# Kernel optimization log

Measured on AMD Instinct MI355X. Metric: run time of the kernel, lower is better.

Reference implementation:

```python
import jax, jax.numpy as jnp
import numpy as np

B, S, H, NH = 2, 2048, 1024, 16
D = H // NH  # per-head dim = 64
NEG = -1000000000.0
EPS = 1e-6


def setup_inputs() -> dict:
    key = jax.random.key(0)
    ks = jax.random.split(key, 8)
    q = jax.random.normal(ks[0], (B, S, H), dtype=jnp.float32)
    k = jax.random.normal(ks[1], (B, S, H), dtype=jnp.float32)
    v = jax.random.normal(ks[2], (B, S, H), dtype=jnp.float32)
    mask = jax.random.randint(ks[3], (B, S, S), 0, 2, dtype=jnp.int32)
    # learned params (torch Linear stores W as [out,in]; y = x @ W.T)
    sc = 1.0 / np.sqrt(H)
    Wq = jax.random.normal(ks[4], (H, H), dtype=jnp.float32) * sc
    Wk = jax.random.normal(ks[5], (H, H), dtype=jnp.float32) * sc
    Wv = jax.random.normal(ks[6], (H, H), dtype=jnp.float32) * sc
    ln_gamma = jnp.ones((H,), dtype=jnp.float32)
    ln_beta = jnp.zeros((H,), dtype=jnp.float32)
    return {"q": q, "k": k, "v": v, "mask": mask,
            "Wq": Wq, "Wk": Wk, "Wv": Wv,
            "ln_gamma": ln_gamma, "ln_beta": ln_beta}


def _mha(q, k, v, mask, Wq, Wk, Wv, ln_gamma, ln_beta):
    residual = q
    # projections: note original never applies self.scale, and self.fc is unused
    qh = (q @ Wq.T).reshape(B, S, NH, D).transpose(0, 2, 1, 3)  # [B,NH,S,D]
    kh = (k @ Wk.T).reshape(B, S, NH, D).transpose(0, 2, 1, 3)
    vh = (v @ Wv.T).reshape(B, S, NH, D).transpose(0, 2, 1, 3)
    scores = jnp.einsum('bhqd,bhkd->bhqk', qh, kh)  # NO 1/sqrt(d) scaling (faithful)
    scores = jnp.where(mask[:, None, :, :] == 0, NEG, scores)
    attn = jax.nn.softmax(scores, axis=-1)
    ctx = jnp.einsum('bhqk,bhkd->bhqd', attn, vh)
    ctx = ctx.transpose(0, 2, 1, 3).reshape(B, S, H)
    ctx = ctx + residual  # dropout = identity in eval
    mu = jnp.mean(ctx, axis=-1, keepdims=True)
    var = jnp.var(ctx, axis=-1, keepdims=True)
    out = (ctx - mu) / jnp.sqrt(var + EPS) * ln_gamma + ln_beta
    return out, attn


def reference(q, k, v, mask, Wq, Wk, Wv, ln_gamma, ln_beta):
    return _mha(q, k, v, mask, Wq, Wk, Wv, ln_gamma, ln_beta)
```

## Files before the change

kernel.cpp:

```cpp
#include <hip/hip_runtime.h>
#include <hip/hip_fp16.h>

typedef _Float16 f16;
typedef _Float16 f16x8 __attribute__((ext_vector_type(8)));
typedef _Float16 f16x4 __attribute__((ext_vector_type(4)));
typedef float    f32x4 __attribute__((ext_vector_type(4)));
typedef float    f32x2 __attribute__((ext_vector_type(2)));

#define NEGV -1000000000.0f

__global__ __launch_bounds__(256) void cvt3(const float* __restrict__ a,
                                            const float* __restrict__ b,
                                            const float* __restrict__ c,
                                            f16* __restrict__ out, int per) {
  const float* src = blockIdx.y == 0 ? a : (blockIdx.y == 1 ? b : c);
  int i = (blockIdx.x * 256 + threadIdx.x) * 4;
  if (i >= per) return;
  f32x4 v = *(const f32x4*)(src + i);
  f16x4 h; h[0]=(f16)v[0]; h[1]=(f16)v[1]; h[2]=(f16)v[2]; h[3]=(f16)v[3];
  *(f16x4*)(out + (size_t)blockIdx.y * per + i) = h;
}

__global__ __launch_bounds__(256) void pack_mask(const int* __restrict__ m,
                                                 unsigned* __restrict__ bits) {
  size_t i = (size_t)blockIdx.x * 256 + threadIdx.x;
  unsigned long long b = __ballot(m[i] != 0);
  int lane = threadIdx.x & 63;
  if (lane == 0)       bits[i >> 5] = (unsigned)b;
  else if (lane == 32) bits[i >> 5] = (unsigned)(b >> 32);
}

__device__ inline void gld16(const void* g, void* l) {
  __builtin_amdgcn_global_load_lds((const __attribute__((address_space(1))) void*)g,
                                   (__attribute__((address_space(3))) void*)l, 16, 0, 0);
}

__global__ __launch_bounds__(256) void gemm_proj(const f16* __restrict__ Xall,
                                                 const f16* __restrict__ Wall,
                                                 f16* __restrict__ Qh,
                                                 f16* __restrict__ Kh,
                                                 f16* __restrict__ Vn) {
  __shared__ f16 lA[4][128][8];
  __shared__ f16 lB[4][128][8];
  const int z = blockIdx.z;
  const f16* A  = Xall + (size_t)z * (4096u * 1024u);
  const f16* Wt = Wall + (size_t)z * (1024u * 1024u);
  f16* Y = (z == 0) ? Qh : (z == 1 ? Kh : Vn);
  const int t = threadIdx.x;
  const int brow = blockIdx.y * 128, bcol = blockIdx.x * 128;
  const int w = t >> 6, l = t & 63;
  const int wr = w >> 1, wc = w & 1;
  const int lr = l & 15, lg = l >> 4;
  f32x4 acc[4][4] = {};

  for (int k0 = 0; k0 < 1024; k0 += 32) {
#pragma unroll
    for (int j = 0; j < 2; j++) {
      const int p = j * 4096 + t * 16;
      const int ks = p >> 11, row = (p >> 4) & 127;
      gld16(A  + (size_t)(brow + row) * 1024 + k0 + ks * 8, (char*)lA + p);
      gld16(Wt + (size_t)(bcol + row) * 1024 + k0 + ks * 8, (char*)lB + p);
    }
    __syncthreads();
    f16x8 af[4], bf[4];
#pragma unroll
    for (int mi = 0; mi < 4; mi++) af[mi] = *(const f16x8*)&lA[lg][wr * 64 + mi * 16 + lr][0];
#pragma unroll
    for (int ni = 0; ni < 4; ni++) bf[ni] = *(const f16x8*)&lB[lg][wc * 64 + ni * 16 + lr][0];
#pragma unroll
    for (int mi = 0; mi < 4; mi++)
#pragma unroll
      for (int ni = 0; ni < 4; ni++)
        acc[mi][ni] = __builtin_amdgcn_mfma_f32_16x16x32_f16(af[mi], bf[ni], acc[mi][ni], 0, 0, 0);
    __syncthreads();
  }

  const int mb0 = brow + wr * 64, nb0 = bcol + wc * 64;
#pragma unroll
  for (int mi = 0; mi < 4; mi++)
#pragma unroll
    for (int ni = 0; ni < 4; ni++)
#pragma unroll
      for (int j = 0; j < 4; j++) {
        const int m = mb0 + mi * 16 + lg * 4 + j;
        const int n = nb0 + ni * 16 + lr;
        const int bb = m >> 11, s = m & 2047;
        const int h = n >> 6, d = n & 63;
        Y[((((size_t)bb * 16 + h) * 2048 + s) << 6) + d] = (f16)acc[mi][ni][j];
      }
}

__global__ __launch_bounds__(512) void transposeV(const f16* __restrict__ Vn,
                                                  f16* __restrict__ VhT) {
  const int bh = blockIdx.y, s0 = blockIdx.x * 64;
  const int t = threadIdx.x, l = t & 63, w = t >> 6;
  const f16x8 v = *(const f16x8*)(Vn + (((size_t)bh * 2048 + s0 + l) << 6) + w * 8);
#pragma unroll
  for (int e = 0; e < 8; e++)
    VhT[(((size_t)bh * 64 + w * 8 + e) << 11) + s0 + l] = v[e];
}

__device__ inline char* swzW(char* wb, int row, int col) {
  return wb + row * 256 + ((col * 2) ^ ((row & 7) << 4));
}

__global__ __launch_bounds__(512, 4) void attn_fused(const f16* __restrict__ Qh,
                                                     const f16* __restrict__ Kh,
                                                     const f16* __restrict__ VhT,
                                                     const unsigned* __restrict__ mbits,
                                                     float* __restrict__ attn,
                                                     float* __restrict__ ctx) {
  __shared__ f16 lK[8][128][8];
  __shared__ f16 lVT[16][64][8];
  __shared__ char Pw[8 * 4096];
  const int wg = blockIdx.x;
  const int bh = (wg >> 1) & 31;
  const int qg = ((wg >> 6) << 1) | (wg & 1);
  const int b = bh >> 4, h = bh & 15;
  const int t = threadIdx.x, w = t >> 6, l = t & 63;
  const int lr = l & 15, lg = l >> 4;
  const int qr = qg * 128 + w * 16;
  char* wb = Pw + w * 4096;

  const int pA = t * 16, pB = 8192 + t * 16;
  const int ksA = pA >> 11, rwA = (pA >> 4) & 127;
  const int ksB = pB >> 11, rwB = (pB >> 4) & 127;
  const int vsA = pA >> 10, vdA = (pA >> 4) & 63;
  const int vsB = pB >> 10, vdB = (pB >> 4) & 63;
  const f16* Kbase = Kh + ((size_t)bh << 17);
  const f16* Vbase = VhT + ((size_t)bh << 17);

  const f16* qp = Qh + (((size_t)bh * 2048 + qr + lr) << 6) + lg * 8;
  const f16x8 aq0 = *(const f16x8*)qp;
  const f16x8 aq1 = *(const f16x8*)(qp + 32);

  const unsigned* mrow0 = mbits + ((size_t)b * 2048 + qr + lg * 4) * 64;

  float sj[4] = {0.f, 0.f, 0.f, 0.f};
  f16x8 kra = *(const f16x8*)(Kbase + ((size_t)rwA << 6) + ksA * 8);
  f16x8 krb = *(const f16x8*)(Kbase + ((size_t)rwB << 6) + ksB * 8);
  for (int t16 = 0; t16 < 16; t16++) {
    const int kb = t16 * 128;
    __syncthreads();
    *(f16x8*)((char*)lK + pA) = kra;
    *(f16x8*)((char*)lK + pB) = krb;
    __syncthreads();
    uint4 mrow[4];
#pragma unroll
    for (int j = 0; j < 4; j++) mrow[j] = *(const uint4*)(mrow0 + j * 64 + (kb >> 5));
    if (t16 < 15) {
      const f16* nb = Kbase + ((size_t)(kb + 128) << 6);
      kra = *(const f16x8*)(nb + ((size_t)rwA << 6) + ksA * 8);
      krb = *(const f16x8*)(nb + ((size_t)rwB << 6) + ksB * 8);
    }
#pragma unroll
    for (int nf = 0; nf < 8; nf++) {
      f32x4 s4 = {};
      s4 = __builtin_amdgcn_mfma_f32_16x16x32_f16(aq0, *(const f16x8*)&lK[lg][nf * 16 + lr][0], s4, 0, 0, 0);
      s4 = __builtin_amdgcn_mfma_f32_16x16x32_f16(aq1, *(const f16x8*)&lK[4 + lg][nf * 16 + lr][0], s4, 0, 0, 0);
      const unsigned bp = ((nf & 1) << 4) + lr;
#pragma unroll
      for (int j = 0; j < 4; j++) {
        const unsigned bit = (((const unsigned*)&mrow[j])[nf >> 1] >> bp) & 1u;
        sj[j] += bit ? __expf(s4[j]) : 0.f;
      }
    }
  }
  float SI[4];
#pragma unroll
  for (int j = 0; j < 4; j++) {
    float s = sj[j];
#pragma unroll
    for (int o = 1; o < 16; o <<= 1) s += __shfl_xor(s, o, 64);
    SI[j] = 1.0f / s;
  }

  f32x4 acc[4] = {};
  kra = *(const f16x8*)(Kbase + ((size_t)rwA << 6) + ksA * 8);
  krb = *(const f16x8*)(Kbase + ((size_t)rwB << 6) + ksB * 8);
  f16x8 vra = *(const f16x8*)(Vbase + ((size_t)vdA << 11) + vsA * 8);
  f16x8 vrb = *(const f16x8*)(Vbase + ((size_t)vdB << 11) + vsB * 8);
  float* abase = attn + (((size_t)bh * 2048 + qr) << 11);
  const int srow = l >> 3, scol = (l & 7) * 4;
  for (int t16 = 0; t16 < 16; t16++) {
    const int kb = t16 * 128;
    __syncthreads();
    *(f16x8*)((char*)lK + pA) = kra;
    *(f16x8*)((char*)lK + pB) = krb;
    *(f16x8*)((char*)lVT + pA) = vra;
    *(f16x8*)((char*)lVT + pB) = vrb;
    __syncthreads();
    uint4 mrow[4];
#pragma unroll
    for (int j = 0; j < 4; j++) mrow[j] = *(const uint4*)(mrow0 + j * 64 + (kb >> 5));
    if (t16 < 15) {
      const f16* nk = Kbase + ((size_t)(kb + 128) << 6);
      kra = *(const f16x8*)(nk + ((size_t)rwA << 6) + ksA * 8);
      krb = *(const f16x8*)(nk + ((size_t)rwB << 6) + ksB * 8);
      const f16* nv = Vbase + kb + 128;
      vra = *(const f16x8*)(nv + ((size_t)vdA << 11) + vsA * 8);
      vrb = *(const f16x8*)(nv + ((size_t)vdB << 11) + vsB * 8);
    }
#pragma unroll
    for (int nf = 0; nf < 8; nf++) {
      f32x4 s4 = {};
      s4 = __builtin_amdgcn_mfma_f32_16x16x32_f16(aq0, *(const f16x8*)&lK[lg][nf * 16 + lr][0], s4, 0, 0, 0);
      s4 = __builtin_amdgcn_mfma_f32_16x16x32_f16(aq1, *(const f16x8*)&lK[4 + lg][nf * 16 + lr][0], s4, 0, 0, 0);
      const unsigned bp = ((nf & 1) << 4) + lr;
#pragma unroll
      for (int j = 0; j < 4; j++) {
        const unsigned bit = (((const unsigned*)&mrow[j])[nf >> 1] >> bp) & 1u;
        const float pj = bit ? __expf(s4[j]) * SI[j] : 0.f;
        *(f16*)swzW(wb, lg * 4 + j, nf * 16 + lr) = (f16)pj;
      }
    }
#pragma unroll
    for (int kk = 0; kk < 4; kk++) {
      const f16x8 pa = *(const f16x8*)swzW(wb, lr, kk * 32 + lg * 8);
#pragma unroll
      for (int nf = 0; nf < 4; nf++)
        acc[nf] = __builtin_amdgcn_mfma_f32_16x16x32_f16(pa, *(const f16x8*)&lVT[kk * 4 + lg][nf * 16 + lr][0], acc[nf], 0, 0, 0);
    }
#pragma unroll
    for (int h2 = 0; h2 < 2; h2++) {
      const int row = srow + h2 * 8;
      float* arow = abase + ((size_t)row << 11) + kb + scol;
#pragma unroll
      for (int u = 0; u < 4; u++) {
        const f16x4 p4 = *(const f16x4*)swzW(wb, row, scol + u * 32);
        f32x4 o;
#pragma unroll
        for (int e = 0; e < 4; e++) o[e] = (float)p4[e];
        *(f32x4*)(arow + u * 32) = o;
      }
    }
  }

#pragma unroll
  for (int nf = 0; nf < 4; nf++)
#pragma unroll
    for (int j = 0; j < 4; j++)
      ctx[((size_t)b * 2048 + qr + lg * 4 + j) * 1024 + h * 64 + nf * 16 + lr] = acc[nf][j];
}

__global__ __launch_bounds__(256) void ln_res(const float* __restrict__ qres,
                                              const float* __restrict__ gamma,
                                              const float* __restrict__ beta,
                                              float* __restrict__ io) {
  const int tok = blockIdx.x;
  const int t = threadIdx.x;
  float* rowp = io + (size_t)tok * 1024;
  const float* qp = qres + (size_t)tok * 1024;
  const f32x4 c = *(const f32x4*)(rowp + t * 4);
  const f32x4 r = *(const f32x4*)(qp + t * 4);
  f32x4 vals;
  float s = 0.f, s2 = 0.f;
#pragma unroll
  for (int e = 0; e < 4; e++) { float x = c[e] + r[e]; vals[e] = x; s += x; s2 += x * x; }
#pragma unroll
  for (int o = 1; o < 64; o <<= 1) { s += __shfl_xor(s, o, 64); s2 += __shfl_xor(s2, o, 64); }
  __shared__ float rs[4][2];
  const int w = t >> 6;
  if ((t & 63) == 0) { rs[w][0] = s; rs[w][1] = s2; }
  __syncthreads();
  s  = rs[0][0] + rs[1][0] + rs[2][0] + rs[3][0];
  s2 = rs[0][1] + rs[1][1] + rs[2][1] + rs[3][1];
  const float mu = s * (1.f / 1024.f);
  const float var = s2 * (1.f / 1024.f) - mu * mu;
  const float rstd = rsqrtf(var + 1e-6f);
  const f32x4 g  = *(const f32x4*)(gamma + t * 4);
  const f32x4 be = *(const f32x4*)(beta + t * 4);
  f32x4 o;
#pragma unroll
  for (int e = 0; e < 4; e++) o[e] = (vals[e] - mu) * rstd * g[e] + be[e];
  *(f32x4*)(rowp + t * 4) = o;
}

extern "C" void kernel_launch(void* const* d_in, const int* in_sizes, int n_in,
                              void* d_out, int out_size, void* d_ws, size_t ws_size,
                              hipStream_t stream) {
  const float* q     = (const float*)d_in[0];
  const float* k     = (const float*)d_in[1];
  const float* v     = (const float*)d_in[2];
  const int*   mask  = (const int*)d_in[3];
  const float* Wq    = (const float*)d_in[4];
  const float* Wk    = (const float*)d_in[5];
  const float* Wv    = (const float*)d_in[6];
  const float* gamma = (const float*)d_in[7];
  const float* beta  = (const float*)d_in[8];
  float* out  = (float*)d_out;
  float* attn = out + (size_t)4194304;
  const size_t MB = 1u << 20;
  char* ws = (char*)d_ws;

  f16 *x16, *W16, *Qh, *Kh, *Vn, *VhT; unsigned* mb;
  if (ws_size >= 63 * MB) {
    x16 = (f16*)ws;              W16 = (f16*)(ws + 24 * MB);
    Qh  = (f16*)(ws + 30 * MB);  Kh  = (f16*)(ws + 38 * MB);
    Vn  = (f16*)(ws + 46 * MB);  VhT = (f16*)(ws + 54 * MB);
    mb  = (unsigned*)(ws + 62 * MB);
  } else {
    x16 = (f16*)attn;            W16 = (f16*)((char*)attn + 24 * MB);
    Vn  = (f16*)((char*)attn + 30 * MB);
    Qh  = (f16*)ws;              Kh  = (f16*)(ws + 8 * MB);
    VhT = (f16*)(ws + 16 * MB);  mb  = (unsigned*)(ws + 24 * MB);
  }

  cvt3<<<dim3(4096, 3), 256, 0, stream>>>(q, k, v, x16, 4194304);
  cvt3<<<dim3(1024, 3), 256, 0, stream>>>(Wq, Wk, Wv, W16, 1048576);
  pack_mask<<<dim3(32768), 256, 0, stream>>>(mask, mb);
  gemm_proj<<<dim3(8, 32, 3), 256, 0, stream>>>(x16, W16, Qh, Kh, Vn);
  transposeV<<<dim3(32, 32), 512, 0, stream>>>(Vn, VhT);
  attn_fused<<<dim3(512), 512, 0, stream>>>(Qh, Kh, VhT, mb, attn, out);
  ln_res<<<dim3(4096), 256, 0, stream>>>(q, gamma, beta, out);
}
```

Baseline: 332.2 us.

## Load K/V MFMA operands directly from global memory, drop LDS staging and barriers

Removes the shared-memory staging of K and V tiles and the two block-wide barriers per iteration. Each wave now reads its MFMA B operands straight from global memory and relies on L2/cache reuse across the eight waves. It also remaps workgroup-to-(batch,head,query-group) indexing so that blocks sharing the same head run close together. This trades LDS traffic and synchronisation for more global/L2 load traffic and exposed load latency with no explicit prefetch.

New measurement: 537.7 us. 61.9% more time.

```diff
diff --git a/kernel.cpp b/kernel.cpp
--- a/kernel.cpp
+++ b/kernel.cpp
@@ -110,23 +110,16 @@
                                                      const unsigned* __restrict__ mbits,
                                                      float* __restrict__ attn,
                                                      float* __restrict__ ctx) {
-  __shared__ f16 lK[8][128][8];
-  __shared__ f16 lVT[16][64][8];
   __shared__ char Pw[8 * 4096];
   const int wg = blockIdx.x;
-  const int bh = (wg >> 1) & 31;
-  const int qg = ((wg >> 6) << 1) | (wg & 1);
+  const int bh = ((wg & 7) << 2) | (wg >> 7);
+  const int qg = (wg >> 3) & 15;
   const int b = bh >> 4, h = bh & 15;
   const int t = threadIdx.x, w = t >> 6, l = t & 63;
   const int lr = l & 15, lg = l >> 4;
   const int qr = qg * 128 + w * 16;
   char* wb = Pw + w * 4096;
 
-  const int pA = t * 16, pB = 8192 + t * 16;
-  const int ksA = pA >> 11, rwA = (pA >> 4) & 127;
-  const int ksB = pB >> 11, rwB = (pB >> 4) & 127;
-  const int vsA = pA >> 10, vdA = (pA >> 4) & 63;
-  const int vsB = pB >> 10, vdB = (pB >> 4) & 63;
   const f16* Kbase = Kh + ((size_t)bh << 17);
   const f16* Vbase = VhT + ((size_t)bh << 17);
 
@@ -137,27 +130,20 @@
   const unsigned* mrow0 = mbits + ((size_t)b * 2048 + qr + lg * 4) * 64;
 
   float sj[4] = {0.f, 0.f, 0.f, 0.f};
-  f16x8 kra = *(const f16x8*)(Kbase + ((size_t)rwA << 6) + ksA * 8);
-  f16x8 krb = *(const f16x8*)(Kbase + ((size_t)rwB << 6) + ksB * 8);
   for (int t16 = 0; t16 < 16; t16++) {
     const int kb = t16 * 128;
-    __syncthreads();
-    *(f16x8*)((char*)lK + pA) = kra;
-    *(f16x8*)((char*)lK + pB) = krb;
-    __syncthreads();
     uint4 mrow[4];
 #pragma unroll
     for (int j = 0; j < 4; j++) mrow[j] = *(const uint4*)(mrow0 + j * 64 + (kb >> 5));
-    if (t16 < 15) {
-      const f16* nb = Kbase + ((size_t)(kb + 128) << 6);
-      kra = *(const f16x8*)(nb + ((size_t)rwA << 6) + ksA * 8);
-      krb = *(const f16x8*)(nb + ((size_t)rwB << 6) + ksB * 8);
-    }
+    const f16* kt = Kbase + ((size_t)(kb + lr) << 6) + lg * 8;
 #pragma unroll
     for (int nf = 0; nf < 8; nf++) {
+      const f16* kp = kt + (nf << 10);
+      const f16x8 bk0 = *(const f16x8*)kp;
+      const f16x8 bk1 = *(const f16x8*)(kp + 32);
       f32x4 s4 = {};
-      s4 = __builtin_amdgcn_mfma_f32_16x16x32_f16(aq0, *(const f16x8*)&lK[lg][nf * 16 + lr][0], s4, 0, 0, 0);
-      s4 = __builtin_amdgcn_mfma_f32_16x16x32_f16(aq1, *(const f16x8*)&lK[4 + lg][nf * 16 + lr][0], s4, 0, 0, 0);
+      s4 = __builtin_amdgcn_mfma_f32_16x16x32_f16(aq0, bk0, s4, 0, 0, 0);
+      s4 = __builtin_amdgcn_mfma_f32_16x16x32_f16(aq1, bk1, s4, 0, 0, 0);
       const unsigned bp = ((nf & 1) << 4) + lr;
 #pragma unroll
       for (int j = 0; j < 4; j++) {
@@ -176,36 +162,22 @@
   }
 
   f32x4 acc[4] = {};
-  kra = *(const f16x8*)(Kbase + ((size_t)rwA << 6) + ksA * 8);
-  krb = *(const f16x8*)(Kbase + ((size_t)rwB << 6) + ksB * 8);
-  f16x8 vra = *(const f16x8*)(Vbase + ((size_t)vdA << 11) + vsA * 8);
-  f16x8 vrb = *(const f16x8*)(Vbase + ((size_t)vdB << 11) + vsB * 8);
   float* abase = attn + (((size_t)bh * 2048 + qr) << 11);
   const int srow = l >> 3, scol = (l & 7) * 4;
   for (int t16 = 0; t16 < 16; t16++) {
     const int kb = t16 * 128;
-    __syncthreads();
-    *(f16x8*)((char*)lK + pA) = kra;
-    *(f16x8*)((char*)lK + pB) = krb;
-    *(f16x8*)((char*)lVT + pA) = vra;
-    *(f16x8*)((char*)lVT + pB) = vrb;
-    __syncthreads();
     uint4 mrow[4];
 #pragma unroll
     for (int j = 0; j < 4; j++) mrow[j] = *(const uint4*)(mrow0 + j * 64 + (kb >> 5));
-    if (t16 < 15) {
-      const f16* nk = Kbase + ((size_t)(kb + 128) << 6);
-      kra = *(const f16x8*)(nk + ((size_t)rwA << 6) + ksA * 8);
-      krb = *(const f16x8*)(nk + ((size_t)rwB << 6) + ksB * 8);
-      const f16* nv = Vbase + kb + 128;
-      vra = *(const f16x8*)(nv + ((size_t)vdA << 11) + vsA * 8);
-      vrb = *(const f16x8*)(nv + ((size_t)vdB << 11) + vsB * 8);
-    }
+    const f16* kt = Kbase + ((size_t)(kb + lr) << 6) + lg * 8;
 #pragma unroll
     for (int nf = 0; nf < 8; nf++) {
+      const f16* kp = kt + (nf << 10);
+      const f16x8 bk0 = *(const f16x8*)kp;
+      const f16x8 bk1 = *(const f16x8*)(kp + 32);
       f32x4 s4 = {};
-      s4 = __builtin_amdgcn_mfma_f32_16x16x32_f16(aq0, *(const f16x8*)&lK[lg][nf * 16 + lr][0], s4, 0, 0, 0);
-      s4 = __builtin_amdgcn_mfma_f32_16x16x32_f16(aq1, *(const f16x8*)&lK[4 + lg][nf * 16 + lr][0], s4, 0, 0, 0);
+      s4 = __builtin_amdgcn_mfma_f32_16x16x32_f16(aq0, bk0, s4, 0, 0, 0);
+      s4 = __builtin_amdgcn_mfma_f32_16x16x32_f16(aq1, bk1, s4, 0, 0, 0);
       const unsigned bp = ((nf & 1) << 4) + lr;
 #pragma unroll
       for (int j = 0; j < 4; j++) {
@@ -218,8 +190,10 @@
     for (int kk = 0; kk < 4; kk++) {
       const f16x8 pa = *(const f16x8*)swzW(wb, lr, kk * 32 + lg * 8);
 #pragma unroll
-      for (int nf = 0; nf < 4; nf++)
-        acc[nf] = __builtin_amdgcn_mfma_f32_16x16x32_f16(pa, *(const f16x8*)&lVT[kk * 4 + lg][nf * 16 + lr][0], acc[nf], 0, 0, 0);
+      for (int nf = 0; nf < 4; nf++) {
+        const f16x8 bv = *(const f16x8*)(Vbase + (((size_t)(nf * 16 + lr)) << 11) + kb + kk * 32 + lg * 8);
+        acc[nf] = __builtin_amdgcn_mfma_f32_16x16x32_f16(pa, bv, acc[nf], 0, 0, 0);
+      }
     }
 #pragma unroll
     for (int h2 = 0; h2 < 2; h2++) {
```

## Split attention into separate sum-exp kernel and PV/attn-write kernel

Applied to the files above, without the earlier changes.

The fused attention kernel ran two passes: first accumulating masked exp sums per row, then computing normalized probabilities, writing attn and doing the PV product. This splits the first pass into its own kernel that stores reciprocal row sums to workspace, and the second kernel reads them. It also changes the block-to-(bh,qg) mapping so consecutive blocks spread across heads. The intent is probably to reduce per-kernel register/LDS pressure or improve scheduling, at the cost of an extra launch and a small workspace round-trip.

Result: faster. 307.3 us (-7.5%).

```diff
diff --git a/kernel.cpp b/kernel.cpp
--- a/kernel.cpp
+++ b/kernel.cpp
@@ -100,22 +100,88 @@
     VhT[(((size_t)bh * 64 + w * 8 + e) << 11) + s0 + l] = v[e];
 }
 
+__global__ __launch_bounds__(512, 4) void sumexp_k(const f16* __restrict__ Qh,
+                                                   const f16* __restrict__ Kh,
+                                                   const unsigned* __restrict__ mbits,
+                                                   float* __restrict__ SIo) {
+  __shared__ f16 lK[8][128][8];
+  const int wg = blockIdx.x;
+  const int bh = ((wg & 7) << 2) | (wg >> 7);
+  const int qg = (wg >> 3) & 15;
+  const int b = bh >> 4;
+  const int t = threadIdx.x, w = t >> 6, l = t & 63;
+  const int lr = l & 15, lg = l >> 4;
+  const int qr = qg * 128 + w * 16;
+
+  const int pA = t * 16, pB = 8192 + t * 16;
+  const int ksA = pA >> 11, rwA = (pA >> 4) & 127;
+  const int ksB = pB >> 11, rwB = (pB >> 4) & 127;
+  const f16* Kbase = Kh + ((size_t)bh << 17);
+
+  const f16* qp = Qh + (((size_t)bh * 2048 + qr + lr) << 6) + lg * 8;
+  const f16x8 aq0 = *(const f16x8*)qp;
+  const f16x8 aq1 = *(const f16x8*)(qp + 32);
+  const unsigned* mrow0 = mbits + ((size_t)b * 2048 + qr + lg * 4) * 64;
+
+  float sj[4] = {0.f, 0.f, 0.f, 0.f};
+  f16x8 kra = *(const f16x8*)(Kbase + ((size_t)rwA << 6) + ksA * 8);
+  f16x8 krb = *(const f16x8*)(Kbase + ((size_t)rwB << 6) + ksB * 8);
+  for (int t16 = 0; t16 < 16; t16++) {
+    const int kb = t16 * 128;
+    __syncthreads();
+    *(f16x8*)((char*)lK + pA) = kra;
+    *(f16x8*)((char*)lK + pB) = krb;
+    __syncthreads();
+    uint4 mrow[4];
+#pragma unroll
+    for (int j = 0; j < 4; j++) mrow[j] = *(const uint4*)(mrow0 + j * 64 + (kb >> 5));
+    if (t16 < 15) {
+      const f16* nb = Kbase + ((size_t)(kb + 128) << 6);
+      kra = *(const f16x8*)(nb + ((size_t)rwA << 6) + ksA * 8);
+      krb = *(const f16x8*)(nb + ((size_t)rwB << 6) + ksB * 8);
+    }
+#pragma unroll
+    for (int nf = 0; nf < 8; nf++) {
+      f32x4 s4 = {};
+      s4 = __builtin_amdgcn_mfma_f32_16x16x32_f16(aq0, *(const f16x8*)&lK[lg][nf * 16 + lr][0], s4, 0, 0, 0);
+      s4 = __builtin_amdgcn_mfma_f32_16x16x32_f16(aq1, *(const f16x8*)&lK[4 + lg][nf * 16 + lr][0], s4, 0, 0, 0);
+      const unsigned bp = ((nf & 1) << 4) + lr;
+#pragma unroll
+      for (int j = 0; j < 4; j++) {
+        const unsigned bit = (((const unsigned*)&mrow[j])[nf >> 1] >> bp) & 1u;
+        sj[j] += bit ? __expf(s4[j]) : 0.f;
+      }
+    }
+  }
+#pragma unroll
+  for (int j = 0; j < 4; j++) {
+#pragma unroll
+    for (int o = 1; o < 16; o <<= 1) sj[j] += __shfl_xor(sj[j], o, 64);
+  }
+  if (lr == 0) {
+    float* o = SIo + ((size_t)bh << 11) + qr + lg * 4;
+    o[0] = 1.0f / sj[0]; o[1] = 1.0f / sj[1];
+    o[2] = 1.0f / sj[2]; o[3] = 1.0f / sj[3];
+  }
+}
+
 __device__ inline char* swzW(char* wb, int row, int col) {
   return wb + row * 256 + ((col * 2) ^ ((row & 7) << 4));
 }
 
-__global__ __launch_bounds__(512, 4) void attn_fused(const f16* __restrict__ Qh,
-                                                     const f16* __restrict__ Kh,
-                                                     const f16* __restrict__ VhT,
-                                                     const unsigned* __restrict__ mbits,
-                                                     float* __restrict__ attn,
-                                                     float* __restrict__ ctx) {
+__global__ __launch_bounds__(512, 4) void attn_pv(const f16* __restrict__ Qh,
+                                                  const f16* __restrict__ Kh,
+                                                  const f16* __restrict__ VhT,
+                                                  const unsigned* __restrict__ mbits,
+                                                  const float* __restrict__ SIo,
+                                                  float* __restrict__ attn,
+                                                  float* __restrict__ ctx) {
   __shared__ f16 lK[8][128][8];
   __shared__ f16 lVT[16][64][8];
   __shared__ char Pw[8 * 4096];
   const int wg = blockIdx.x;
-  const int bh = (wg >> 1) & 31;
-  const int qg = ((wg >> 6) << 1) | (wg & 1);
+  const int bh = ((wg & 7) << 2) | (wg >> 7);
+  const int qg = (wg >> 3) & 15;
   const int b = bh >> 4, h = bh & 15;
   const int t = threadIdx.x, w = t >> 6, l = t & 63;
   const int lr = l & 15, lg = l >> 4;
@@ -133,51 +199,15 @@
   const f16* qp = Qh + (((size_t)bh * 2048 + qr + lr) << 6) + lg * 8;
   const f16x8 aq0 = *(const f16x8*)qp;
   const f16x8 aq1 = *(const f16x8*)(qp + 32);
-
   const unsigned* mrow0 = mbits + ((size_t)b * 2048 + qr + lg * 4) * 64;
 
-  float sj[4] = {0.f, 0.f, 0.f, 0.f};
+  float SI[4];
+#pragma unroll
+  for (int j = 0; j < 4; j++) SI[j] = SIo[((size_t)bh << 11) + qr + lg * 4 + j];
+
+  f32x4 acc[4] = {};
   f16x8 kra = *(const f16x8*)(Kbase + ((size_t)rwA << 6) + ksA * 8);
   f16x8 krb = *(const f16x8*)(Kbase + ((size_t)rwB << 6) + ksB * 8);
-  for (int t16 = 0; t16 < 16; t16++) {
-    const int kb = t16 * 128;
-    __syncthreads();
-    *(f16x8*)((char*)lK + pA) = kra;
-    *(f16x8*)((char*)lK + pB) = krb;
-    __syncthreads();
-    uint4 mrow[4];
-#pragma unroll
-    for (int j = 0; j < 4; j++) mrow[j] = *(const uint4*)(mrow0 + j * 64 + (kb >> 5));
-    if (t16 < 15) {
-      const f16* nb = Kbase + ((size_t)(kb + 128) << 6);
-      kra = *(const f16x8*)(nb + ((size_t)rwA << 6) + ksA * 8);
-      krb = *(const f16x8*)(nb + ((size_t)rwB << 6) + ksB * 8);
-    }
-#pragma unroll
-    for (int nf = 0; nf < 8; nf++) {
-      f32x4 s4 = {};
-      s4 = __builtin_amdgcn_mfma_f32_16x16x32_f16(aq0, *(const f16x8*)&lK[lg][nf * 16 + lr][0], s4, 0, 0, 0);
-      s4 = __builtin_amdgcn_mfma_f32_16x16x32_f16(aq1, *(const f16x8*)&lK[4 + lg][nf * 16 + lr][0], s4, 0, 0, 0);
-      const unsigned bp = ((nf & 1) << 4) + lr;
-#pragma unroll
-      for (int j = 0; j < 4; j++) {
-        const unsigned bit = (((const unsigned*)&mrow[j])[nf >> 1] >> bp) & 1u;
-        sj[j] += bit ? __expf(s4[j]) : 0.f;
-      }
-    }
-  }
-  float SI[4];
-#pragma unroll
-  for (int j = 0; j < 4; j++) {
-    float s = sj[j];
-#pragma unroll
-    for (int o = 1; o < 16; o <<= 1) s += __shfl_xor(s, o, 64);
-    SI[j] = 1.0f / s;
-  }
-
-  f32x4 acc[4] = {};
-  kra = *(const f16x8*)(Kbase + ((size_t)rwA << 6) + ksA * 8);
-  krb = *(const f16x8*)(Kbase + ((size_t)rwB << 6) + ksB * 8);
   f16x8 vra = *(const f16x8*)(Vbase + ((size_t)vdA << 11) + vsA * 8);
   f16x8 vrb = *(const f16x8*)(Vbase + ((size_t)vdB << 11) + vsB * 8);
   float* abase = attn + (((size_t)bh * 2048 + qr) << 11);
@@ -293,17 +323,19 @@
   const size_t MB = 1u << 20;
   char* ws = (char*)d_ws;
 
-  f16 *x16, *W16, *Qh, *Kh, *Vn, *VhT; unsigned* mb;
-  if (ws_size >= 63 * MB) {
+  f16 *x16, *W16, *Qh, *Kh, *Vn, *VhT; unsigned* mb; float* SIo;
+  if (ws_size >= 65 * MB) {
     x16 = (f16*)ws;              W16 = (f16*)(ws + 24 * MB);
     Qh  = (f16*)(ws + 30 * MB);  Kh  = (f16*)(ws + 38 * MB);
     Vn  = (f16*)(ws + 46 * MB);  VhT = (f16*)(ws + 54 * MB);
     mb  = (unsigned*)(ws + 62 * MB);
+    SIo = (float*)(ws + 63 * MB);
   } else {
     x16 = (f16*)attn;            W16 = (f16*)((char*)attn + 24 * MB);
     Vn  = (f16*)((char*)attn + 30 * MB);
     Qh  = (f16*)ws;              Kh  = (f16*)(ws + 8 * MB);
     VhT = (f16*)(ws + 16 * MB);  mb  = (unsigned*)(ws + 24 * MB);
+    SIo = (float*)(ws + 25 * MB);
   }
 
   cvt3<<<dim3(4096, 3), 256, 0, stream>>>(q, k, v, x16, 4194304);
@@ -311,6 +343,7 @@
   pack_mask<<<dim3(32768), 256, 0, stream>>>(mask, mb);
   gemm_proj<<<dim3(8, 32, 3), 256, 0, stream>>>(x16, W16, Qh, Kh, Vn);
   transposeV<<<dim3(32, 32), 512, 0, stream>>>(Vn, VhT);
-  attn_fused<<<dim3(512), 512, 0, stream>>>(Qh, Kh, VhT, mb, attn, out);
+  sumexp_k<<<dim3(512), 512, 0, stream>>>(Qh, Kh, mb, SIo);
+  attn_pv<<<dim3(512), 512, 0, stream>>>(Qh, Kh, VhT, mb, SIo, attn, out);
   ln_res<<<dim3(4096), 256, 0, stream>>>(q, gamma, beta, out);
 }
```
